# Optimization experiments

Measured on AMD Instinct MI355X. Metric: run time of the kernel, lower is better.

The kernel has to match this reference:

```python
import jax, jax.numpy as jnp
import numpy as np

B, S, D = 4, 2048, 1024
H = 16
HD = D // H  # 64


def setup_inputs() -> dict:
    key = jax.random.key(0)
    ks = jax.random.split(key, 6)
    scale = 1.0 / np.sqrt(D)
    return {
        "x": jax.random.normal(ks[0], (B, S, D), dtype=jnp.float32),
        "W_q": jax.random.normal(ks[1], (D, D), dtype=jnp.float32) * scale,
        "W_k": jax.random.normal(ks[2], (D, D), dtype=jnp.float32) * scale,
        "W_v": jax.random.normal(ks[3], (D, D), dtype=jnp.float32) * scale,
        "W_o": jax.random.normal(ks[4], (D, D), dtype=jnp.float32) * scale,
        "b_o": jax.random.normal(ks[5], (D,), dtype=jnp.float32) * 0.01,
    }


def reference(x, W_q, W_k, W_v, W_o, b_o):
    b, n, _ = x.shape
    # projections (Linear stores weight as [out,in]; here W_* are [in,out])
    q = (x @ W_q).reshape(b, n, H, HD).transpose(0, 2, 1, 3)  # [b,h,n,hd]
    k = (x @ W_k).reshape(b, n, H, HD).transpose(0, 2, 1, 3)
    v = (x @ W_v).reshape(b, n, H, HD).transpose(0, 2, 1, 3)
    scores = jnp.einsum("bhqd,bhkd->bhqk", q, k) / np.sqrt(HD).astype(np.float32)
    causal = jnp.tril(jnp.ones((n, n), dtype=bool))  # True = keep
    scores = jnp.where(causal, scores, -jnp.inf)
    weights = jax.nn.softmax(scores, axis=-1)
    ctx = jnp.einsum("bhqk,bhkd->bhqd", weights, v)
    ctx = ctx.transpose(0, 2, 1, 3).reshape(b, n, D)
    return ctx @ W_o + b_o
```

## Files before the change

kernel.cpp:

```cpp
#include <hip/hip_runtime.h>
#include <cstdint>

#define S_LEN 2048
#define D_MODEL 1024
#define NH 16
#define HDIM 64
#define BATCH 4

typedef __attribute__((ext_vector_type(8))) __bf16 bfrag;
typedef __attribute__((ext_vector_type(4))) float ffrag;

__device__ __forceinline__ unsigned short f2bf(float f) {
    union { float f; uint32_t u; } v; v.f = f;
    uint32_t u = v.u;
    u += 0x7fff + ((u >> 16) & 1);
    return (unsigned short)(u >> 16);
}

__device__ __forceinline__ bfrag ld_frag(const unsigned short* p) {
    union { uint4 u; bfrag b; } x;
    x.u = *(const uint4*)p;
    return x.b;
}

__device__ __forceinline__ float fast_exp2(float x) {
#if __has_builtin(__builtin_amdgcn_exp2f)
    return __builtin_amdgcn_exp2f(x);
#else
    return __expf(x * 0.6931471805599453f);
#endif
}

__device__ __forceinline__ uint32_t pack_bf16(float a, float b) {
    union { float f; uint32_t u; } x, y; x.f = a; y.f = b;
    return __builtin_amdgcn_perm(y.u + 0x8000u, x.u + 0x8000u, 0x07060302u);
}

__device__ __forceinline__ void g2l16(const unsigned short* g, unsigned short* l) {
    __builtin_amdgcn_global_load_lds(
        (const __attribute__((address_space(1))) void*)g,
        (__attribute__((address_space(3))) void*)l, 16, 0, 0);
}

__global__ __launch_bounds__(256) void cast_x_kernel(const float* __restrict__ x,
                                                     unsigned short* __restrict__ xb,
                                                     int n8) {
    int i = blockIdx.x * 256 + threadIdx.x;
    if (i >= n8) return;
    const float4* p = (const float4*)x + (size_t)i * 2;
    float4 a = p[0], b = p[1];
    union { unsigned short u[8]; uint4 v; } o;
    o.u[0]=f2bf(a.x); o.u[1]=f2bf(a.y); o.u[2]=f2bf(a.z); o.u[3]=f2bf(a.w);
    o.u[4]=f2bf(b.x); o.u[5]=f2bf(b.y); o.u[6]=f2bf(b.z); o.u[7]=f2bf(b.w);
    ((uint4*)xb)[i] = o.v;
}

__global__ __launch_bounds__(256) void transpose_w_kernel(const float* __restrict__ w0,
                                                          const float* __restrict__ w1,
                                                          const float* __restrict__ w2,
                                                          const float* __restrict__ w3,
                                                          unsigned short* __restrict__ wt) {
    __shared__ float tile[32][33];
    int mat = blockIdx.z;
    const float* w = (mat == 0) ? w0 : (mat == 1) ? w1 : (mat == 2) ? w2 : w3;
    int n0 = blockIdx.x * 32, k0 = blockIdx.y * 32;
    int tx = threadIdx.x, ty = threadIdx.y;
    for (int i = 0; i < 32; i += 8)
        tile[ty + i][tx] = w[(size_t)(k0 + ty + i) * D_MODEL + n0 + tx];
    __syncthreads();
    unsigned short* o = wt + (size_t)mat * D_MODEL * D_MODEL;
    for (int i = 0; i < 32; i += 8)
        o[(size_t)(n0 + ty + i) * D_MODEL + (k0 + tx)] = f2bf(tile[tx][ty + i]);
}

__global__ __launch_bounds__(256) void gemm_kernel(
    const unsigned short* __restrict__ A,
    const unsigned short* __restrict__ Bt,
    int mode,
    unsigned short* __restrict__ Qb,
    unsigned short* __restrict__ Kb,
    unsigned short* __restrict__ Vtb,
    float* __restrict__ Out,
    const float* __restrict__ bias) {
    __shared__ unsigned short As[128 * 32];
    __shared__ unsigned short Bs[128 * 32];
    int t = threadIdx.x;
    int m0 = blockIdx.y * 128;
    int n0 = blockIdx.x * 128;
    int wave = t >> 6, lane = t & 63;
    int quad = lane >> 4, lrow = lane & 15;
    int wm = (wave & 1) * 64, wn = (wave >> 1) * 64;

    ffrag acc[4][4];
    const ffrag fz = {0.f, 0.f, 0.f, 0.f};
    for (int i = 0; i < 4; i++)
        for (int j = 0; j < 4; j++) acc[i][j] = fz;

    int c0 = t, c1 = 256 + t;
    int r0 = c0 >> 2, cg0 = (c0 & 3) ^ ((r0 >> 1) & 3);
    int r1 = c1 >> 2, cg1 = (c1 & 3) ^ ((r1 >> 1) & 3);
    const unsigned short* A0 = A + (size_t)(m0 + r0) * D_MODEL + cg0 * 8;
    const unsigned short* A1 = A + (size_t)(m0 + r1) * D_MODEL + cg1 * 8;
    const unsigned short* B0 = Bt + (size_t)(n0 + r0) * D_MODEL + cg0 * 8;
    const unsigned short* B1 = Bt + (size_t)(n0 + r1) * D_MODEL + cg1 * 8;
    unsigned short* lA0 = &As[(wave * 64) * 8];
    unsigned short* lA1 = &As[(256 + wave * 64) * 8];
    unsigned short* lB0 = &Bs[(wave * 64) * 8];
    unsigned short* lB1 = &Bs[(256 + wave * 64) * 8];

    for (int k0 = 0; k0 < D_MODEL; k0 += 32) {
        g2l16(A0 + k0, lA0);
        g2l16(A1 + k0, lA1);
        g2l16(B0 + k0, lB0);
        g2l16(B1 + k0, lB1);
        __syncthreads();
        bfrag af[4], bf[4];
        for (int mi = 0; mi < 4; mi++) {
            int row = wm + mi * 16 + lrow;
            af[mi] = ld_frag(&As[row * 32 + ((quad ^ ((row >> 1) & 3)) * 8)]);
        }
        for (int ni = 0; ni < 4; ni++) {
            int row = wn + ni * 16 + lrow;
            bf[ni] = ld_frag(&Bs[row * 32 + ((quad ^ ((row >> 1) & 3)) * 8)]);
        }
        for (int mi = 0; mi < 4; mi++)
            for (int ni = 0; ni < 4; ni++)
                acc[mi][ni] = __builtin_amdgcn_mfma_f32_16x16x32_bf16(af[mi], bf[ni], acc[mi][ni], 0, 0, 0);
        __syncthreads();
    }

    for (int mi = 0; mi < 4; mi++) {
        int row = m0 + wm + mi * 16 + quad * 4;
        for (int ni = 0; ni < 4; ni++) {
            int col = n0 + wn + ni * 16 + lrow;
            for (int r = 0; r < 4; r++) {
                float v = acc[mi][ni][r];
                int m = row + r;
                if (mode == 0) {
                    int matid = col >> 10;
                    int nn = col & 1023;
                    int h = nn >> 6, d = nn & 63;
                    int b = m >> 11, s = m & 2047;
                    size_t bh = (size_t)(b * NH + h);
                    if (matid == 0)      Qb[(bh * S_LEN + s) * HDIM + d] = f2bf(v);
                    else if (matid == 1) Kb[(bh * S_LEN + s) * HDIM + d] = f2bf(v);
                    else                 Vtb[(bh * HDIM + d) * S_LEN + s] = f2bf(v);
                } else {
                    Out[(size_t)m * D_MODEL + col] = v + bias[col];
                }
            }
        }
    }
}

#define SCALE2 0.18033688f
#define CSHIFT 4.0f
#define KVBUF 4096

__global__ __launch_bounds__(256, 4) void attn_kernel(
    const unsigned short* __restrict__ Qb,
    const unsigned short* __restrict__ Kb,
    const unsigned short* __restrict__ Vtb,
    unsigned short* __restrict__ ctxb) {
    __shared__ unsigned short Ks[2 * KVBUF];
    __shared__ unsigned short Vs[2 * KVBUF];
    __shared__ unsigned short Ps[4 * 32 * 64];
    int bx = blockIdx.x;
    int bh = blockIdx.y;
    int t = threadIdx.x;
    int wave = t >> 6, lane = t & 63;
    int quad = lane >> 4, lrow = lane & 15;
    int swz = lrow & 7;
    int ca = (quad ^ swz) * 8;
    int cb = ca ^ 32;

    const unsigned short* Qg = Qb + (size_t)bh * S_LEN * HDIM;
    const unsigned short* Kg = Kb + (size_t)bh * S_LEN * HDIM;
    const unsigned short* Vg = Vtb + (size_t)bh * HDIM * S_LEN;
    int b = bh >> 4, h = bh & 15;

    int c0 = t, c1 = 256 + t;
    int kr0 = c0 >> 3, kp0 = (c0 & 7) ^ (kr0 & 7);
    int kr1 = c1 >> 3, kp1 = (c1 & 7) ^ (kr1 & 7);
    const unsigned short* pK0 = Kg + (size_t)kr0 * HDIM + kp0 * 8;
    const unsigned short* pK1 = Kg + (size_t)kr1 * HDIM + kp1 * 8;
    const unsigned short* pV0 = Vg + (size_t)kr0 * S_LEN + kp0 * 8;
    const unsigned short* pV1 = Vg + (size_t)kr1 * S_LEN + kp1 * 8;
    unsigned short* lK0 = &Ks[(wave * 64) * 8];
    unsigned short* lK1 = &Ks[(256 + wave * 64) * 8];
    unsigned short* lV0 = &Vs[(wave * 64) * 8];
    unsigned short* lV1 = &Vs[(256 + wave * 64) * 8];
    unsigned short* Pw = &Ps[wave * 32 * 64];

    for (int ph = 0; ph < 2; ph++) {
        int qbi = ph == 0 ? (15 - bx) : bx;
        int qw = qbi * 128 + wave * 32;
        int qw_u = __builtin_amdgcn_readfirstlane(qw);
        int nk = 2 * qbi + 2;

        bfrag qf[2][2];
#pragma unroll
        for (int g = 0; g < 2; g++)
#pragma unroll
            for (int c = 0; c < 2; c++)
                qf[g][c] = ld_frag(Qg + (size_t)(qw + g * 16 + lrow) * HDIM + c * 32 + quad * 8);

        ffrag acc[2][4];
        const ffrag fz = {0.f, 0.f, 0.f, 0.f};
#pragma unroll
        for (int g = 0; g < 2; g++)
#pragma unroll
            for (int d = 0; d < 4; d++) acc[g][d] = fz;
        float l_i[2] = {0.f, 0.f};

        __syncthreads();
        g2l16(pK0, lK0);
        g2l16(pK1, lK1);
        g2l16(pV0, lV0);
        g2l16(pV1, lV1);

        for (int kt = 0; kt < nk; kt++) {
            int kbase = kt * 64;
            int buf = (kt & 1) * KVBUF;
            __syncthreads();
            if (kt + 1 < nk) {
                int nb = ((kt + 1) & 1) * KVBUF;
                size_t krow_off = (size_t)(kbase + 64) * HDIM;
                g2l16(pK0 + krow_off, lK0 + nb);
                g2l16(pK1 + krow_off, lK1 + nb);
                g2l16(pV0 + kbase + 64, lV0 + nb);
                g2l16(pV1 + kbase + 64, lV1 + nb);
            }

            if (kbase > qw_u + 31) continue;

#pragma unroll
            for (int g = 0; g < 2; g++) {
                if (kbase > qw_u + g * 16 + 15) continue;
                ffrag sf[4];
#pragma unroll
                for (int ki = 0; ki < 4; ki++) {
                    int krow = buf + (ki * 16 + lrow) * 64;
                    bfrag ka = ld_frag(&Ks[krow + ca]);
                    bfrag kb = ld_frag(&Ks[krow + cb]);
                    ffrag s = fz;
                    s = __builtin_amdgcn_mfma_f32_16x16x32_bf16(ka, qf[g][0], s, 0, 0, 0);
                    s = __builtin_amdgcn_mfma_f32_16x16x32_bf16(kb, qf[g][1], s, 0, 0, 0);
                    sf[ki] = s;
                }

                int qg = qw + g * 16 + lrow;
                bool need_mask = (kbase + 63) > (qw_u + g * 16);
                float sv[16];
                float rsum = 0.f;
#pragma unroll
                for (int ki = 0; ki < 4; ki++)
#pragma unroll
                    for (int r = 0; r < 4; r++) {
                        float v = sf[ki][r];
                        if (need_mask) {
                            int key = kbase + ki * 16 + quad * 4 + r;
                            v = (key <= qg) ? v : -3.0e38f;
                        }
                        float p = fast_exp2(__builtin_fmaf(v, SCALE2, -CSHIFT));
                        sv[ki * 4 + r] = p;
                        rsum += p;
                    }
                rsum += __shfl_xor(rsum, 16);
                rsum += __shfl_xor(rsum, 32);
                l_i[g] += rsum;
                int prow = (g * 16 + lrow) * 64;
#pragma unroll
                for (int ki = 0; ki < 4; ki++) {
                    uint2 w2;
                    w2.x = pack_bf16(sv[ki * 4 + 0], sv[ki * 4 + 1]);
                    w2.y = pack_bf16(sv[ki * 4 + 2], sv[ki * 4 + 3]);
                    int pc = ((ki * 2 + (quad >> 1)) ^ swz) * 8 + (quad & 1) * 4;
                    *(uint2*)&Pw[prow + pc] = w2;
                }
            }

            bfrag pf[2][2];
#pragma unroll
            for (int g = 0; g < 2; g++) {
                if (kbase > qw_u + g * 16 + 15) continue;
                int prow = (g * 16 + lrow) * 64;
                pf[g][0] = ld_frag(&Pw[prow + ca]);
                pf[g][1] = ld_frag(&Pw[prow + cb]);
            }
#pragma unroll
            for (int di = 0; di < 4; di++) {
                int vrow = buf + (di * 16 + lrow) * 64;
                bfrag va = ld_frag(&Vs[vrow + ca]);
                bfrag vb = ld_frag(&Vs[vrow + cb]);
#pragma unroll
                for (int g = 0; g < 2; g++) {
                    if (kbase > qw_u + g * 16 + 15) continue;
                    acc[g][di] = __builtin_amdgcn_mfma_f32_16x16x32_bf16(va, pf[g][0], acc[g][di], 0, 0, 0);
                    acc[g][di] = __builtin_amdgcn_mfma_f32_16x16x32_bf16(vb, pf[g][1], acc[g][di], 0, 0, 0);
                }
            }
        }

#pragma unroll
        for (int g = 0; g < 2; g++) {
            float rl = __builtin_amdgcn_rcpf(l_i[g]);
#pragma unroll
            for (int di = 0; di < 4; di++) {
                uint2 w2;
                w2.x = pack_bf16(acc[g][di][0] * rl, acc[g][di][1] * rl);
                w2.y = pack_bf16(acc[g][di][2] * rl, acc[g][di][3] * rl);
                *(uint2*)&Pw[lrow * 72 + di * 16 + quad * 4] = w2;
            }
            int ql = lane >> 3, cc = lane & 7;
#pragma unroll
            for (int p = 0; p < 2; p++) {
                uint4 vv = *(uint4*)&Pw[(p * 8 + ql) * 72 + cc * 8];
                int q = qw + g * 16 + p * 8 + ql;
                *(uint4*)(ctxb + ((size_t)b * S_LEN + q) * D_MODEL + h * HDIM + cc * 8) = vv;
            }
        }
    }
}

extern "C" void kernel_launch(void* const* d_in, const int* in_sizes, int n_in,
                              void* d_out, int out_size, void* d_ws, size_t ws_size,
                              hipStream_t stream) {
    const float* x   = (const float*)d_in[0];
    const float* W_q = (const float*)d_in[1];
    const float* W_k = (const float*)d_in[2];
    const float* W_v = (const float*)d_in[3];
    const float* W_o = (const float*)d_in[4];
    const float* b_o = (const float*)d_in[5];
    float* out = (float*)d_out;

    unsigned short* xb   = (unsigned short*)d_ws;
    unsigned short* Wt   = xb + (size_t)8192 * 1024;
    unsigned short* Qb   = Wt + (size_t)4 * 1024 * 1024;
    unsigned short* Kb   = Qb + (size_t)64 * 2048 * 64;
    unsigned short* Vtb  = Kb + (size_t)64 * 2048 * 64;
    unsigned short* ctxb = Vtb + (size_t)64 * 2048 * 64;
    unsigned short* Wto  = Wt + (size_t)3 * 1024 * 1024;

    int n8 = (BATCH * S_LEN * D_MODEL) / 8;
    cast_x_kernel<<<n8 / 256, 256, 0, stream>>>(x, xb, n8);
    transpose_w_kernel<<<dim3(32, 32, 4), dim3(32, 8), 0, stream>>>(W_q, W_k, W_v, W_o, Wt);
    gemm_kernel<<<dim3(24, 64), 256, 0, stream>>>(xb, Wt, 0, Qb, Kb, Vtb, nullptr, nullptr);
    attn_kernel<<<dim3(8, 64), 256, 0, stream>>>(Qb, Kb, Vtb, ctxb);
    gemm_kernel<<<dim3(8, 64), 256, 0, stream>>>(ctxb, Wto, 1, nullptr, nullptr, nullptr, out, b_o);
}
```

Before: 295.8 us.

## Double-buffer GEMM LDS tiles and write V row-major with separate transpose

The projection/output GEMM now double-buffers its LDS tiles, prefetching the next K-slice while computing the current one, and drops one barrier per iteration. V is written in row-major [bh,s,d] layout instead of a strided transposed scatter, and a new small kernel transposes it into the Vt layout used by attention. This targets load latency in the GEMM main loop and uncoalesced stores in the epilogue. It costs twice the LDS per block and an extra kernel launch plus one read-write pass over V.

```diff
diff --git a/kernel.cpp b/kernel.cpp
--- a/kernel.cpp
+++ b/kernel.cpp
@@ -73,17 +73,39 @@
         o[(size_t)(n0 + ty + i) * D_MODEL + (k0 + tx)] = f2bf(tile[tx][ty + i]);
 }
 
+__global__ __launch_bounds__(256) void transpose_v_kernel(const unsigned short* __restrict__ Vb,
+                                                          unsigned short* __restrict__ Vtb) {
+    __shared__ unsigned short tile[64][72];
+    int st = blockIdx.x;
+    int bh = blockIdx.y;
+    int t = threadIdx.x;
+    int sl = t >> 2, dc = (t & 3) * 16;
+    const unsigned short* src = Vb + ((size_t)bh * S_LEN + st * 64 + sl) * HDIM + dc;
+    *(uint4*)&tile[sl][dc]     = *(const uint4*)(src);
+    *(uint4*)&tile[sl][dc + 8] = *(const uint4*)(src + 8);
+    __syncthreads();
+    int d = t >> 2, sc = (t & 3) * 16;
+    union { unsigned short u[16]; uint4 v[2]; } o;
+#pragma unroll
+    for (int i = 0; i < 16; i++) o.u[i] = tile[sc + i][d];
+    unsigned short* dst = Vtb + ((size_t)bh * HDIM + d) * S_LEN + st * 64 + sc;
+    *(uint4*)(dst)     = o.v[0];
+    *(uint4*)(dst + 8) = o.v[1];
+}
+
+#define GBUF 4096
+
 __global__ __launch_bounds__(256) void gemm_kernel(
     const unsigned short* __restrict__ A,
     const unsigned short* __restrict__ Bt,
     int mode,
     unsigned short* __restrict__ Qb,
     unsigned short* __restrict__ Kb,
-    unsigned short* __restrict__ Vtb,
+    unsigned short* __restrict__ Vb,
     float* __restrict__ Out,
     const float* __restrict__ bias) {
-    __shared__ unsigned short As[128 * 32];
-    __shared__ unsigned short Bs[128 * 32];
+    __shared__ unsigned short As[2 * GBUF];
+    __shared__ unsigned short Bs[2 * GBUF];
     int t = threadIdx.x;
     int m0 = blockIdx.y * 128;
     int n0 = blockIdx.x * 128;
@@ -108,25 +130,33 @@
     unsigned short* lB0 = &Bs[(wave * 64) * 8];
     unsigned short* lB1 = &Bs[(256 + wave * 64) * 8];
 
+    g2l16(A0, lA0);
+    g2l16(A1, lA1);
+    g2l16(B0, lB0);
+    g2l16(B1, lB1);
+
     for (int k0 = 0; k0 < D_MODEL; k0 += 32) {
-        g2l16(A0 + k0, lA0);
-        g2l16(A1 + k0, lA1);
-        g2l16(B0 + k0, lB0);
-        g2l16(B1 + k0, lB1);
+        int buf = ((k0 >> 5) & 1) * GBUF;
         __syncthreads();
+        if (k0 + 32 < D_MODEL) {
+            int nb = (((k0 >> 5) + 1) & 1) * GBUF;
+            g2l16(A0 + k0 + 32, lA0 + nb);
+            g2l16(A1 + k0 + 32, lA1 + nb);
+            g2l16(B0 + k0 + 32, lB0 + nb);
+            g2l16(B1 + k0 + 32, lB1 + nb);
+        }
         bfrag af[4], bf[4];
         for (int mi = 0; mi < 4; mi++) {
             int row = wm + mi * 16 + lrow;
-            af[mi] = ld_frag(&As[row * 32 + ((quad ^ ((row >> 1) & 3)) * 8)]);
+            af[mi] = ld_frag(&As[buf + row * 32 + ((quad ^ ((row >> 1) & 3)) * 8)]);
         }
         for (int ni = 0; ni < 4; ni++) {
             int row = wn + ni * 16 + lrow;
-            bf[ni] = ld_frag(&Bs[row * 32 + ((quad ^ ((row >> 1) & 3)) * 8)]);
+            bf[ni] = ld_frag(&Bs[buf + row * 32 + ((quad ^ ((row >> 1) & 3)) * 8)]);
         }
         for (int mi = 0; mi < 4; mi++)
             for (int ni = 0; ni < 4; ni++)
                 acc[mi][ni] = __builtin_amdgcn_mfma_f32_16x16x32_bf16(af[mi], bf[ni], acc[mi][ni], 0, 0, 0);
-        __syncthreads();
     }
 
     for (int mi = 0; mi < 4; mi++) {
@@ -144,7 +174,7 @@
                     size_t bh = (size_t)(b * NH + h);
                     if (matid == 0)      Qb[(bh * S_LEN + s) * HDIM + d] = f2bf(v);
                     else if (matid == 1) Kb[(bh * S_LEN + s) * HDIM + d] = f2bf(v);
-                    else                 Vtb[(bh * HDIM + d) * S_LEN + s] = f2bf(v);
+                    else                 Vb[(bh * S_LEN + s) * HDIM + d] = f2bf(v);
                 } else {
                     Out[(size_t)m * D_MODEL + col] = v + bias[col];
                 }
@@ -340,12 +370,14 @@
     unsigned short* Kb   = Qb + (size_t)64 * 2048 * 64;
     unsigned short* Vtb  = Kb + (size_t)64 * 2048 * 64;
     unsigned short* ctxb = Vtb + (size_t)64 * 2048 * 64;
+    unsigned short* Vb   = ctxb;
     unsigned short* Wto  = Wt + (size_t)3 * 1024 * 1024;
 
     int n8 = (BATCH * S_LEN * D_MODEL) / 8;
     cast_x_kernel<<<n8 / 256, 256, 0, stream>>>(x, xb, n8);
     transpose_w_kernel<<<dim3(32, 32, 4), dim3(32, 8), 0, stream>>>(W_q, W_k, W_v, W_o, Wt);
-    gemm_kernel<<<dim3(24, 64), 256, 0, stream>>>(xb, Wt, 0, Qb, Kb, Vtb, nullptr, nullptr);
+    gemm_kernel<<<dim3(24, 64), 256, 0, stream>>>(xb, Wt, 0, Qb, Kb, Vb, nullptr, nullptr);
+    transpose_v_kernel<<<dim3(32, 64), 256, 0, stream>>>(Vb, Vtb);
     attn_kernel<<<dim3(8, 64), 256, 0, stream>>>(Qb, Kb, Vtb, ctxb);
     gemm_kernel<<<dim3(8, 64), 256, 0, stream>>>(ctxb, Wto, 1, nullptr, nullptr, nullptr, out, b_o);
 }
```

New measurement: 299.0 us. Within noise of the previous version (+1.1%).
